# Kernel optimization log

Hardware: AMD Instinct MI355X
Metric: run time of the kernel (lower is better)

Reference implementation:

```python
import jax, jax.numpy as jnp
import numpy as np

BN_EPS = 1e-5


def setup_inputs() -> dict:
    key = jax.random.key(0)
    ks = jax.random.split(key, 8)
    B, C, H, W = 8, 256, 48, 48
    s = 1.0 / np.sqrt(C)
    x = jax.random.normal(ks[0], (B, C, H, W), dtype=jnp.float32)
    Wk = jax.random.normal(ks[1], (C, C), dtype=jnp.float32) * s
    Wq = jax.random.normal(ks[2], (C, C), dtype=jnp.float32) * s
    Wv = jax.random.normal(ks[3], (C, C), dtype=jnp.float32) * s
    W2 = jax.random.normal(ks[4], (C, C), dtype=jnp.float32) * s
    b2 = jax.random.normal(ks[5], (C,), dtype=jnp.float32) * 0.02
    gamma = jnp.ones((C,), dtype=jnp.float32)
    beta = jnp.zeros((C,), dtype=jnp.float32)
    return {"x": x, "Wk": Wk, "Wq": Wq, "Wv": Wv, "W2": W2, "b2": b2,
            "gamma": gamma, "beta": beta}


def reference(x, Wk, Wq, Wv, W2, b2, gamma, beta):
    B, C, H, W = x.shape
    N = H * W
    xf = x.reshape(B, C, N)
    # 1x1 convs == channel mixing matmuls
    k = jnp.einsum('oc,bcn->bon', Wk, xf)  # (B,C,N)
    q = jnp.einsum('oc,bcn->bon', Wq, xf)  # (B,C,N)
    v = jnp.einsum('oc,bcn->bon', Wv, xf)  # (B,C,N)
    # scores[b,n,m] = sum_c k[b,c,n] * q[b,c,m]  (unscaled, as in source)
    scores = jnp.einsum('bcn,bcm->bnm', k, q)          # (B,N,N)
    prob = jax.nn.softmax(scores, axis=2)
    # out[b,c,n] = sum_m prob[b,n,m] * v[b,c,m]
    attn = jnp.einsum('bnm,bcm->bcn', prob, v).reshape(B, C, H, W)
    # react2: 1x1 conv (with bias) + BatchNorm2d (training-mode batch stats)
    y = jnp.einsum('oc,bchw->bohw', W2, attn) + b2[None, :, None, None]
    mean = jnp.mean(y, axis=(0, 2, 3))
    var = jnp.var(y, axis=(0, 2, 3))  # biased, matches torch BN normalization
    yhat = (y - mean[None, :, None, None]) * jax.lax.rsqrt(var + BN_EPS)[None, :, None, None]
    return yhat * gamma[None, :, None, None] + beta[None, :, None, None]
```

## Files before the change

kernel.cpp:

```cpp
#include <hip/hip_runtime.h>
#include <hip/hip_fp16.h>
#include <math.h>

#define BN_EPS 1e-5f

typedef unsigned short ushort_t;
typedef unsigned int uint_t;

constexpr int BB   = 8;
constexpr int CC   = 256;
constexpr int NN   = 2304;
constexpr int MTOT = BB * NN;
constexpr int NSPLIT = 4;
constexpr int MT32 = 72;
constexpr int TPS  = 18;
constexpr int TILE = 8192;
constexpr float MFIX = 64.0f;
constexpr size_t SZE = (size_t)BB * NN * CC;

typedef short bf16x8 __attribute__((ext_vector_type(8)));
typedef _Float16 f16x8 __attribute__((ext_vector_type(8)));
typedef float f32x16 __attribute__((ext_vector_type(16)));

union F4 { float4 v; float f[4]; };
union US4 { ushort_t u[4]; uint2 v; };
union U4H8 { uint4 v; ushort_t h[8]; };

__device__ __forceinline__ ushort_t f2bf(float f) {
  uint_t u = __float_as_uint(f);
  uint_t r = u + 0x7FFFu + ((u >> 16) & 1u);
  return (ushort_t)(r >> 16);
}
__device__ __forceinline__ float bf2f(ushort_t h) {
  return __uint_as_float(((uint_t)h) << 16);
}
__device__ __forceinline__ ushort_t f2h(float f) {
  return __half_as_ushort(__float2half(f));
}
__device__ __forceinline__ uint_t pk_trunc(float lo, float hi) {
  return __builtin_amdgcn_perm(__float_as_uint(hi), __float_as_uint(lo), 0x07060302u);
}
__device__ __forceinline__ int rowmap(int reg, int laneHi) {
  return (reg & 3) + 8 * (reg >> 2) + 4 * laneHi;
}

__global__ __launch_bounds__(256) void xpose(
    const float* __restrict__ x, ushort_t* __restrict__ xh, ushort_t* __restrict__ xl)
{
  const int b = blockIdx.z, n0 = blockIdx.y * 64, c0 = blockIdx.x * 64;
  __shared__ float t_s[64][67];
  const int tid = threadIdx.x;
#pragma unroll
  for (int t = 0; t < 4; ++t) {
    int e4 = tid + t * 256;
    int r = e4 >> 4, c4 = e4 & 15;
    F4 v; v.v = *(const float4*)&x[((size_t)b * CC + c0 + r) * NN + n0 + c4 * 4];
#pragma unroll
    for (int k = 0; k < 4; ++k) t_s[r][c4 * 4 + k] = v.f[k];
  }
  __syncthreads();
#pragma unroll
  for (int t = 0; t < 4; ++t) {
    int e = tid + t * 256;
    int nr = e >> 4, cc = e & 15;
    US4 hv, lv;
#pragma unroll
    for (int k = 0; k < 4; ++k) {
      const float v = t_s[cc * 4 + k][nr];
      const ushort_t h = f2bf(v);
      hv.u[k] = h;
      lv.u[k] = f2bf(v - bf2f(h));
    }
    const size_t o = ((size_t)b * NN + n0 + nr) * CC + c0 + cc * 4;
    *(uint2*)&xh[o] = hv.v;
    *(uint2*)&xl[o] = lv.v;
  }
}

__global__ __launch_bounds__(256) void wsplit(
    const float* __restrict__ Wk, const float* __restrict__ Wq,
    const float* __restrict__ Wv, const float* __restrict__ W2,
    ushort_t* __restrict__ wh, ushort_t* __restrict__ wl,
    float* __restrict__ stats)
{
  if (blockIdx.x < 2) stats[blockIdx.x * 256 + threadIdx.x] = 0.f;
  const int mat = blockIdx.x >> 5;
  const int off = ((blockIdx.x & 31) * 256 + threadIdx.x) * 8;
  const float* Wm = (mat == 0) ? Wk : (mat == 1) ? Wq : (mat == 2) ? Wv : W2;
  F4 a, c;
  a.v = *(const float4*)&Wm[off];
  c.v = *(const float4*)&Wm[off + 4];
  U4H8 hv, lv;
#pragma unroll
  for (int j = 0; j < 8; ++j) {
    const float v = (j < 4) ? a.f[j] : c.f[j - 4];
    const ushort_t h = f2bf(v);
    hv.h[j] = h;
    lv.h[j] = f2bf(v - bf2f(h));
  }
  *(uint4*)&wh[mat * 65536 + off] = hv.v;
  *(uint4*)&wl[mat * 65536 + off] = lv.v;
}

__global__ __launch_bounds__(256, 2) void qkv_mfma(
    const ushort_t* __restrict__ xh, const ushort_t* __restrict__ xl,
    const ushort_t* __restrict__ wh, const ushort_t* __restrict__ wl,
    ushort_t* __restrict__ kf, ushort_t* __restrict__ qf,
    ushort_t* __restrict__ vt2)
{
  const int mt = blockIdx.x, mat = blockIdx.y, b = blockIdx.z;
  const int tid = threadIdx.x, w = tid >> 6, lane = tid & 63;
  const int l31 = lane & 31, lH = lane >> 5, h8 = lH * 8;
  __shared__ alignas(16) ushort_t vscr[4][32 * 40];

  const int n0 = mt * 32;
  const size_t boff = (size_t)b * NN * CC;

  bf16x8 Xh[16], Xl[16];
  const ushort_t* xhp = xh + boff + (size_t)(n0 + l31) * CC + h8;
  const ushort_t* xlp = xl + boff + (size_t)(n0 + l31) * CC + h8;
#pragma unroll
  for (int kc = 0; kc < 16; ++kc) {
    Xh[kc] = *(const bf16x8*)&xhp[kc * 16];
    Xl[kc] = *(const bf16x8*)&xlp[kc * 16];
  }
  const ushort_t* whm = wh + mat * 65536;
  const ushort_t* wlm = wl + mat * 65536;
  const size_t tbase = (size_t)(b * MT32 + mt) * TILE;

#pragma unroll
  for (int ot = 0; ot < 2; ++ot) {
    const int o0 = w * 64 + ot * 32;
    f32x16 accA = {}, accB = {}, accC = {};
#pragma unroll
    for (int kc = 0; kc < 16; ++kc) {
      bf16x8 Bh = *(const bf16x8*)&whm[(size_t)(o0 + l31) * CC + kc * 16 + h8];
      bf16x8 Bl = *(const bf16x8*)&wlm[(size_t)(o0 + l31) * CC + kc * 16 + h8];
      accA = __builtin_amdgcn_mfma_f32_32x32x16_bf16(Xh[kc], Bh, accA, 0, 0, 0);
      accB = __builtin_amdgcn_mfma_f32_32x32x16_bf16(Xh[kc], Bl, accB, 0, 0, 0);
      accC = __builtin_amdgcn_mfma_f32_32x32x16_bf16(Xl[kc], Bh, accC, 0, 0, 0);
    }
    if (mat < 2) {
#pragma unroll
      for (int reg = 0; reg < 16; ++reg)
        vscr[w][rowmap(reg, lH) * 40 + l31] = f2h(accA[reg] + accB[reg] + accC[reg]);
      ushort_t* ob = ((mat == 0) ? kf : qf) + tbase;
#pragma unroll
      for (int k2 = 0; k2 < 2; ++k2) {
        const int idx = k2 * 64 + lane;
        const int n = idx >> 2, coct = idx & 3;
        uint4 pk = *(const uint4*)&vscr[w][n * 40 + coct * 8];
        *(uint4*)&ob[(size_t)(((o0 >> 3) + coct) * 32 + n) * 8] = pk;
      }
    } else {
#pragma unroll
      for (int reg = 0; reg < 16; ++reg)
        vscr[w][l31 * 40 + rowmap(reg, lH)] = f2bf(accA[reg] + accB[reg] + accC[reg]);
#pragma unroll
      for (int k2 = 0; k2 < 2; ++k2) {
        const int idx = k2 * 64 + lane;
        const int cl = idx >> 2, moct = idx & 3;
        uint4 pk = *(const uint4*)&vscr[w][cl * 40 + moct * 8];
        *(uint4*)&vt2[tbase + (size_t)(moct * 256 + o0 + cl) * 8] = pk;
      }
    }
  }
}

__global__ __launch_bounds__(256, 2) void attn_fused(
    const ushort_t* __restrict__ kf, const ushort_t* __restrict__ qf,
    const ushort_t* __restrict__ vt2,
    ushort_t* __restrict__ Opart, float* __restrict__ Ls)
{
  const int id = blockIdx.x + 18 * (blockIdx.y + 4 * blockIdx.z);
  const int xcd = id & 7, s = id >> 3;
  const int g = xcd * 4 + s / 18;
  const int n0 = (s % 18) * 128;
  const int split = g & 3, b = g >> 2;

  const int tid = threadIdx.x;
  const int w = tid >> 6, lane = tid & 63;
  const int l31 = lane & 31, lH = lane >> 5;

  __shared__ alignas(16) ushort_t sQ[2 * TILE];
  __shared__ alignas(16) ushort_t sV[2 * TILE];
  __shared__ alignas(16) ushort_t sPt[4 * 1280];
  ushort_t* Pt = sPt + w * 1280;

  const ushort_t* qtb = qf + (size_t)(b * MT32 + split * TPS) * TILE;
  const ushort_t* vtb = vt2 + (size_t)(b * MT32 + split * TPS) * TILE;

  f16x8 Kf[16];
  {
    const ushort_t* kt = kf + (size_t)(b * MT32 + (n0 >> 5) + w) * TILE;
#pragma unroll
    for (int kc = 0; kc < 16; ++kc)
      Kf[kc] = *(const f16x8*)&kt[(size_t)((kc * 2 + lH) * 32 + l31) * 8];
  }
  f32x16 O[8];
#pragma unroll
  for (int i = 0; i < 8; ++i) O[i] = (f32x16){};
  float rsum = 0.f;

#define ISSUE_TILE(tt, buf)                                                        \
  {                                                                                \
    const ushort_t* qs = qtb + (size_t)(tt) * TILE;                                \
    const ushort_t* vs = vtb + (size_t)(tt) * TILE;                                \
    ushort_t* ldq = sQ + (buf) * TILE;                                             \
    ushort_t* ldv = sV + (buf) * TILE;                                             \
    _Pragma("unroll")                                                              \
    for (int j = 0; j < 4; ++j) {                                                  \
      const int i = w * 4 + j;                                                     \
      __builtin_amdgcn_global_load_lds(                                            \
          (const __attribute__((address_space(1))) uint_t*)(qs + i * 512 + lane * 8), \
          (__attribute__((address_space(3))) uint_t*)(ldq + i * 512), 16, 0, 0);   \
      __builtin_amdgcn_global_load_lds(                                            \
          (const __attribute__((address_space(1))) uint_t*)(vs + i * 512 + lane * 8), \
          (__attribute__((address_space(3))) uint_t*)(ldv + i * 512), 16, 0, 0);   \
    }                                                                              \
  }

  ISSUE_TILE(0, 0)
  ISSUE_TILE(1, 1)
  __syncthreads();

  for (int t = 0; t < TPS; ++t) {
    const int cur = t & 1;
    const ushort_t* Qs = sQ + cur * TILE;
    const ushort_t* Vs = sV + cur * TILE;
    f32x16 acc = {};
#pragma unroll
    for (int kc = 0; kc < 16; ++kc) {
      f16x8 Aq = *(const f16x8*)&Qs[(size_t)((kc * 2 + lH) * 32 + l31) * 8];
      acc = __builtin_amdgcn_mfma_f32_32x32x16_f16(Aq, Kf[kc], acc, 0, 0, 0);
    }
#pragma unroll
    for (int j = 0; j < 4; ++j) {
      float p0 = __expf(acc[4 * j]     - MFIX);
      float p1 = __expf(acc[4 * j + 1] - MFIX);
      float p2 = __expf(acc[4 * j + 2] - MFIX);
      float p3 = __expf(acc[4 * j + 3] - MFIX);
      rsum += (p0 + p1) + (p2 + p3);
      uint2 pk;
      pk.x = pk_trunc(p0, p1);
      pk.y = pk_trunc(p2, p3);
      *(uint2*)&Pt[l31 * 40 + 8 * j + 4 * lH] = pk;
    }
#pragma unroll
    for (int ks = 0; ks < 2; ++ks) {
      bf16x8 Bp = *(const bf16x8*)&Pt[l31 * 40 + ks * 16 + lH * 8];
#pragma unroll
      for (int cg = 0; cg < 8; ++cg) {
        bf16x8 Av = *(const bf16x8*)&Vs[(size_t)((ks * 2 + lH) * 256 + cg * 32 + l31) * 8];
        O[cg] = __builtin_amdgcn_mfma_f32_32x32x16_bf16(Av, Bp, O[cg], 0, 0, 0);
      }
    }
    __syncthreads();
    if (t + 2 < TPS) ISSUE_TILE(t + 2, cur)
  }
#undef ISSUE_TILE

  ushort_t* Ob = Opart + (size_t)(split * BB + b) * CC * NN;
  const int n = n0 + w * 32 + l31;
#pragma unroll
  for (int cg = 0; cg < 8; ++cg)
#pragma unroll
    for (int reg = 0; reg < 16; ++reg) {
      const int c = cg * 32 + rowmap(reg, lH);
      Ob[(size_t)c * NN + n] = f2bf(O[cg][reg]);
    }
  rsum += __shfl_xor(rsum, 32);
  if (lH == 0)
    Ls[(size_t)split * MTOT + b * NN + n] = rsum;
}

__global__ __launch_bounds__(256, 2) void proj_f(
    const ushort_t* __restrict__ Opart, const float* __restrict__ Ls,
    const ushort_t* __restrict__ w2h, const ushort_t* __restrict__ w2l,
    const float* __restrict__ b2,
    ushort_t* __restrict__ yb, float* __restrict__ stats)
{
  const int mt = blockIdx.x;
  const int tid = threadIdx.x, w = tid >> 6, lane = tid & 63;
  const int l31 = lane & 31, lH = lane >> 5, h8 = lH * 8;
  const int r0 = mt * 32;
  const int b = r0 / NN, nb = r0 % NN;

  __shared__ alignas(16) ushort_t t_s[32 * 264];
  __shared__ float inv_s[32];

  if (tid < 32) {
    float L = 0.f;
#pragma unroll
    for (int sp = 0; sp < NSPLIT; ++sp) L += Ls[(size_t)sp * MTOT + r0 + tid];
    inv_s[tid] = 1.0f / L;
  }
  __syncthreads();

  const size_t obase = ((size_t)b * CC) * NN + nb;
#pragma unroll
  for (int k = 0; k < 4; ++k) {
    const int c = (tid >> 2) + k * 64;
    const int noct = tid & 3;
    float accv[8] = {};
#pragma unroll
    for (int sp = 0; sp < NSPLIT; ++sp) {
      U4H8 pk;
      pk.v = *(const uint4*)&Opart[(size_t)sp * SZE + obase + (size_t)c * NN + noct * 8];
#pragma unroll
      for (int j = 0; j < 8; ++j) accv[j] += bf2f(pk.h[j]);
    }
#pragma unroll
    for (int j = 0; j < 8; ++j) {
      const int nl = noct * 8 + j;
      t_s[nl * 264 + c] = f2bf(accv[j] * inv_s[nl]);
    }
  }
  __syncthreads();

  bf16x8 Af[16];
#pragma unroll
  for (int kc = 0; kc < 16; ++kc)
    Af[kc] = *(const bf16x8*)&t_s[l31 * 264 + kc * 16 + h8];

#pragma unroll
  for (int ot = 0; ot < 2; ++ot) {
    const int o0 = w * 64 + ot * 32;
    f32x16 accA = {}, accB = {};
#pragma unroll
    for (int kc = 0; kc < 16; ++kc) {
      bf16x8 Bh = *(const bf16x8*)&w2h[(size_t)(o0 + l31) * CC + kc * 16 + h8];
      bf16x8 Bl = *(const bf16x8*)&w2l[(size_t)(o0 + l31) * CC + kc * 16 + h8];
      accA = __builtin_amdgcn_mfma_f32_32x32x16_bf16(Af[kc], Bh, accA, 0, 0, 0);
      accB = __builtin_amdgcn_mfma_f32_32x32x16_bf16(Af[kc], Bl, accB, 0, 0, 0);
    }
    const float bj = b2[o0 + l31];
    float cs = 0.f, cq = 0.f;
#pragma unroll
    for (int reg = 0; reg < 16; ++reg) {
      const float v = accA[reg] + accB[reg] + bj;
      yb[(size_t)(r0 + rowmap(reg, lH)) * CC + o0 + l31] = f2bf(v);
      cs += v;
      cq += v * v;
    }
    cs += __shfl_xor(cs, 32);
    cq += __shfl_xor(cq, 32);
    if (lane < 32) {
      atomicAdd(&stats[o0 + l31], cs);
      atomicAdd(&stats[CC + o0 + l31], cq);
    }
  }
}

__global__ __launch_bounds__(256) void bn_out(
    const ushort_t* __restrict__ yb, const float* __restrict__ stats,
    const float* __restrict__ gamma, const float* __restrict__ beta,
    float* __restrict__ out)
{
  const int b = blockIdx.z, n0 = blockIdx.y * 64, c0 = blockIdx.x * 64;
  __shared__ alignas(16) ushort_t t_s[64 * 72];
  __shared__ float aa[64], bbf[64];
  const int tid = threadIdx.x;
  if (tid < 64) {
    const int c = c0 + tid;
    const float mean = stats[c] * (1.0f / MTOT);
    const float var  = stats[CC + c] * (1.0f / MTOT) - mean * mean;
    const float rstd = rsqrtf(var + BN_EPS);
    const float a = rstd * gamma[c];
    aa[tid]  = a;
    bbf[tid] = beta[c] - mean * a;
  }
#pragma unroll
  for (int t = 0; t < 2; ++t) {
    const int e = tid + t * 256;
    const int r = e >> 3, c8 = e & 7;
    const int sc8 = c8 ^ (r & 7);
    *(uint4*)&t_s[r * 72 + sc8 * 8] =
        *(const uint4*)&yb[((size_t)b * NN + n0 + r) * CC + c0 + c8 * 8];
  }
  __syncthreads();
#pragma unroll
  for (int t = 0; t < 4; ++t) {
    const int e4 = tid + t * 256;
    const int cr = e4 >> 4, r4 = e4 & 15;
    const float a = aa[cr], bb2 = bbf[cr];
    F4 o4;
#pragma unroll
    for (int k = 0; k < 4; ++k) {
      const int r = r4 * 4 + k;
      const int idx = r * 72 + (((cr >> 3) ^ (r & 7)) << 3) + (cr & 7);
      o4.f[k] = bf2f(t_s[idx]) * a + bb2;
    }
    *(float4*)&out[((size_t)b * CC + c0 + cr) * NN + n0 + r4 * 4] = o4.v;
  }
}

extern "C" void kernel_launch(void* const* d_in, const int* in_sizes, int n_in,
                              void* d_out, int out_size, void* d_ws, size_t ws_size,
                              hipStream_t stream)
{
  (void)in_sizes; (void)n_in; (void)out_size; (void)ws_size;
  const float* x     = (const float*)d_in[0];
  const float* Wk    = (const float*)d_in[1];
  const float* Wq    = (const float*)d_in[2];
  const float* Wv    = (const float*)d_in[3];
  const float* W2    = (const float*)d_in[4];
  const float* b2    = (const float*)d_in[5];
  const float* gamma = (const float*)d_in[6];
  const float* beta  = (const float*)d_in[7];
  float* out = (float*)d_out;

  ushort_t* u   = (ushort_t*)d_ws;
  ushort_t* xh  = u;
  ushort_t* xl  = u + SZE;
  ushort_t* kf  = u + 2 * SZE;
  ushort_t* qf  = u + 3 * SZE;
  ushort_t* vt2 = u + 4 * SZE;
  ushort_t* Opart = u + 5 * SZE;
  ushort_t* wh  = u + (5 + NSPLIT) * SZE;
  ushort_t* wl  = wh + 4 * 65536;
  float* Ls    = (float*)(wl + 4 * 65536);
  float* stats = Ls + (size_t)NSPLIT * MTOT;
  ushort_t* yb = u;

  xpose     <<<dim3(4, 36, 8),       256, 0, stream>>>(x, xh, xl);
  wsplit    <<<dim3(128),            256, 0, stream>>>(Wk, Wq, Wv, W2, wh, wl, stats);
  qkv_mfma  <<<dim3(72, 3, 8),       256, 0, stream>>>(xh, xl, wh, wl, kf, qf, vt2);
  attn_fused<<<dim3(18, NSPLIT, 8),  256, 0, stream>>>(kf, qf, vt2, Opart, Ls);
  proj_f    <<<dim3(576),            256, 0, stream>>>(Opart, Ls, wh + 3 * 65536,
                                                       wl + 3 * 65536, b2, yb, stats);
  bn_out    <<<dim3(4, 36, 8),       256, 0, stream>>>(yb, stats, gamma, beta, out);
}
```

Measured before the change: 278.7 us.

## Retile QKV projection into 64x128 LDS-staged tiles via direct global-to-LDS loads

The QKV projection kernel changes from one block per 32 rows, with weights read straight from global memory by each wave, to 64-row by 128-output tiles. X and W hi/lo slices are staged into shared memory with global_load_lds over four K steps, and each wave computes a 32x64 sub-tile. This is meant to raise data reuse of weights and activations across waves and cut redundant global and L2 traffic. In exchange it adds syncs per K step with no double buffering, uses about 48KB of LDS, and changes the grid shape and launch bounds.

```diff
diff --git a/kernel.cpp b/kernel.cpp
--- a/kernel.cpp
+++ b/kernel.cpp
@@ -102,65 +102,115 @@
   *(uint4*)&wl[mat * 65536 + off] = lv.v;
 }
 
-__global__ __launch_bounds__(256, 2) void qkv_mfma(
+__global__ __launch_bounds__(256, 3) void qkv_mfma(
     const ushort_t* __restrict__ xh, const ushort_t* __restrict__ xl,
     const ushort_t* __restrict__ wh, const ushort_t* __restrict__ wl,
     ushort_t* __restrict__ kf, ushort_t* __restrict__ qf,
     ushort_t* __restrict__ vt2)
 {
-  const int mt = blockIdx.x, mat = blockIdx.y, b = blockIdx.z;
+  const int mb  = blockIdx.x;
+  const int mat = blockIdx.y >> 1;
+  const int nh  = blockIdx.y & 1;
+  const int b   = blockIdx.z;
   const int tid = threadIdx.x, w = tid >> 6, lane = tid & 63;
-  const int l31 = lane & 31, lH = lane >> 5, h8 = lH * 8;
-  __shared__ alignas(16) ushort_t vscr[4][32 * 40];
-
-  const int n0 = mt * 32;
-  const size_t boff = (size_t)b * NN * CC;
-
-  bf16x8 Xh[16], Xl[16];
-  const ushort_t* xhp = xh + boff + (size_t)(n0 + l31) * CC + h8;
-  const ushort_t* xlp = xl + boff + (size_t)(n0 + l31) * CC + h8;
-#pragma unroll
-  for (int kc = 0; kc < 16; ++kc) {
-    Xh[kc] = *(const bf16x8*)&xhp[kc * 16];
-    Xl[kc] = *(const bf16x8*)&xlp[kc * 16];
-  }
+  const int l31 = lane & 31, lH = lane >> 5;
+  const int wm = w & 1, wn = w >> 1;
+
+  __shared__ alignas(16) ushort_t smem[24576];
+
+  const size_t xrow = ((size_t)b * NN + mb * 64 + lane) * CC;
+  const int obase = nh * 128;
+  const size_t wrow = (size_t)(obase + lane) * CC;
   const ushort_t* whm = wh + mat * 65536;
   const ushort_t* wlm = wl + mat * 65536;
+
+  f32x16 accA[2], accB[2], accC[2];
+#pragma unroll
+  for (int i = 0; i < 2; ++i) {
+    accA[i] = (f32x16){}; accB[i] = (f32x16){}; accC[i] = (f32x16){};
+  }
+
+#define STAGE(k0)                                                                   \
+  {                                                                                 \
+    _Pragma("unroll")                                                               \
+    for (int cc = 0; cc < 2; ++cc) {                                                \
+      const int ch = 2 * w + cc;                                                    \
+      const size_t gx = xrow + (k0) + ch * 8;                                       \
+      __builtin_amdgcn_global_load_lds(                                             \
+          (const __attribute__((address_space(1))) uint_t*)(xh + gx),               \
+          (__attribute__((address_space(3))) uint_t*)(smem + ch * 512), 16, 0, 0);  \
+      __builtin_amdgcn_global_load_lds(                                             \
+          (const __attribute__((address_space(1))) uint_t*)(xl + gx),               \
+          (__attribute__((address_space(3))) uint_t*)(smem + 4096 + ch * 512),      \
+          16, 0, 0);                                                                \
+      _Pragma("unroll")                                                             \
+      for (int h = 0; h < 2; ++h) {                                                 \
+        const size_t gw = wrow + (size_t)h * 64 * CC + (k0) + ch * 8;               \
+        __builtin_amdgcn_global_load_lds(                                           \
+            (const __attribute__((address_space(1))) uint_t*)(whm + gw),            \
+            (__attribute__((address_space(3))) uint_t*)(smem + 8192 + ch * 1024 +   \
+                                                        h * 512), 16, 0, 0);        \
+        __builtin_amdgcn_global_load_lds(                                           \
+            (const __attribute__((address_space(1))) uint_t*)(wlm + gw),            \
+            (__attribute__((address_space(3))) uint_t*)(smem + 16384 + ch * 1024 +  \
+                                                        h * 512), 16, 0, 0);        \
+      }                                                                             \
+    }                                                                               \
+  }
+
+#pragma unroll
+  for (int t = 0; t < 4; ++t) {
+    if (t) __syncthreads();
+    STAGE(t * 64)
+    __syncthreads();
+#pragma unroll
+    for (int kc = 0; kc < 4; ++kc) {
+      const int ch = kc * 2 + lH;
+      const bf16x8 Ah = *(const bf16x8*)&smem[(ch * 64 + wm * 32 + l31) * 8];
+      const bf16x8 Al = *(const bf16x8*)&smem[4096 + (ch * 64 + wm * 32 + l31) * 8];
+#pragma unroll
+      for (int ot = 0; ot < 2; ++ot) {
+        const int oL = wn * 64 + ot * 32 + l31;
+        const bf16x8 Bh = *(const bf16x8*)&smem[8192 + (ch * 128 + oL) * 8];
+        const bf16x8 Bl = *(const bf16x8*)&smem[16384 + (ch * 128 + oL) * 8];
+        accA[ot] = __builtin_amdgcn_mfma_f32_32x32x16_bf16(Ah, Bh, accA[ot], 0, 0, 0);
+        accB[ot] = __builtin_amdgcn_mfma_f32_32x32x16_bf16(Ah, Bl, accB[ot], 0, 0, 0);
+        accC[ot] = __builtin_amdgcn_mfma_f32_32x32x16_bf16(Al, Bh, accC[ot], 0, 0, 0);
+      }
+    }
+  }
+#undef STAGE
+  __syncthreads();
+
+  ushort_t* vscr = smem + w * 1280;
+  const int mt = mb * 2 + wm;
   const size_t tbase = (size_t)(b * MT32 + mt) * TILE;
-
 #pragma unroll
   for (int ot = 0; ot < 2; ++ot) {
-    const int o0 = w * 64 + ot * 32;
-    f32x16 accA = {}, accB = {}, accC = {};
-#pragma unroll
-    for (int kc = 0; kc < 16; ++kc) {
-      bf16x8 Bh = *(const bf16x8*)&whm[(size_t)(o0 + l31) * CC + kc * 16 + h8];
-      bf16x8 Bl = *(const bf16x8*)&wlm[(size_t)(o0 + l31) * CC + kc * 16 + h8];
-      accA = __builtin_amdgcn_mfma_f32_32x32x16_bf16(Xh[kc], Bh, accA, 0, 0, 0);
-      accB = __builtin_amdgcn_mfma_f32_32x32x16_bf16(Xh[kc], Bl, accB, 0, 0, 0);
-      accC = __builtin_amdgcn_mfma_f32_32x32x16_bf16(Xl[kc], Bh, accC, 0, 0, 0);
-    }
+    const int o0 = obase + wn * 64 + ot * 32;
     if (mat < 2) {
 #pragma unroll
       for (int reg = 0; reg < 16; ++reg)
-        vscr[w][rowmap(reg, lH) * 40 + l31] = f2h(accA[reg] + accB[reg] + accC[reg]);
+        vscr[rowmap(reg, lH) * 40 + l31] =
+            f2h(accA[ot][reg] + accB[ot][reg] + accC[ot][reg]);
       ushort_t* ob = ((mat == 0) ? kf : qf) + tbase;
 #pragma unroll
       for (int k2 = 0; k2 < 2; ++k2) {
         const int idx = k2 * 64 + lane;
         const int n = idx >> 2, coct = idx & 3;
-        uint4 pk = *(const uint4*)&vscr[w][n * 40 + coct * 8];
+        uint4 pk = *(const uint4*)&vscr[n * 40 + coct * 8];
         *(uint4*)&ob[(size_t)(((o0 >> 3) + coct) * 32 + n) * 8] = pk;
       }
     } else {
 #pragma unroll
       for (int reg = 0; reg < 16; ++reg)
-        vscr[w][l31 * 40 + rowmap(reg, lH)] = f2bf(accA[reg] + accB[reg] + accC[reg]);
+        vscr[l31 * 40 + rowmap(reg, lH)] =
+            f2bf(accA[ot][reg] + accB[ot][reg] + accC[ot][reg]);
 #pragma unroll
       for (int k2 = 0; k2 < 2; ++k2) {
         const int idx = k2 * 64 + lane;
         const int cl = idx >> 2, moct = idx & 3;
-        uint4 pk = *(const uint4*)&vscr[w][cl * 40 + moct * 8];
+        uint4 pk = *(const uint4*)&vscr[cl * 40 + moct * 8];
         *(uint4*)&vt2[tbase + (size_t)(moct * 256 + o0 + cl) * 8] = pk;
       }
     }
@@ -425,7 +475,7 @@
 
   xpose     <<<dim3(4, 36, 8),       256, 0, stream>>>(x, xh, xl);
   wsplit    <<<dim3(128),            256, 0, stream>>>(Wk, Wq, Wv, W2, wh, wl, stats);
-  qkv_mfma  <<<dim3(72, 3, 8),       256, 0, stream>>>(xh, xl, wh, wl, kf, qf, vt2);
+  qkv_mfma  <<<dim3(36, 6, 8),       256, 0, stream>>>(xh, xl, wh, wl, kf, qf, vt2);
   attn_fused<<<dim3(18, NSPLIT, 8),  256, 0, stream>>>(kf, qf, vt2, Opart, Ls);
   proj_f    <<<dim3(576),            256, 0, stream>>>(Opart, Ls, wh + 3 * 65536,
                                                        wl + 3 * 65536, b2, yb, stats);
```

Result: faster. 247.1 us (-11.4%).
